# Kernel tuning notes

Hardware: AMD Instinct MI355X
Metric: run time of the kernel (lower is better)

The kernel has to match this reference:

```python
import jax, jax.numpy as jnp
import numpy as np

T, D, E, H, O = 65536, 256, 8, 512, 256
TOP_P = 0.7


def setup_inputs() -> dict:
    key = jax.random.key(0)
    ks = jax.random.split(key, 7)
    s = 0.02
    return {
        "x": jax.random.normal(ks[0], (T, D), dtype=jnp.float32),
        "gate_w": jax.random.normal(ks[1], (D, E), dtype=jnp.float32) * s,
        "gate_b": jnp.zeros((E,), dtype=jnp.float32),
        "w1": jax.random.normal(ks[2], (E, D, H), dtype=jnp.float32) * s,
        "b1": jnp.zeros((E, H), dtype=jnp.float32),
        "w2": jax.random.normal(ks[3], (E, H, O), dtype=jnp.float32) * s,
        "b2": jnp.zeros((E, O), dtype=jnp.float32),
    }


def top_sample(probs, top_p):
    # sort descending, cumsum, keep while cumulative prob <= top_p (always keep top-1)
    order = jnp.argsort(-probs, axis=-1)                       # [T, E]
    probs_sorted = jnp.take_along_axis(probs, order, axis=-1)
    cum = jnp.cumsum(probs_sorted, axis=-1)
    mask = cum <= top_p
    mask = mask.at[:, 0].set(True)
    inv = jnp.argsort(order, axis=-1)                          # unsort permutation
    return jnp.take_along_axis(mask, inv, axis=-1)             # [T, E] bool


def reference(x, gate_w, gate_b, w1, b1, w2, b2):
    logits = x @ gate_w + gate_b                               # [T, E]
    probs = jax.nn.softmax(logits, axis=-1)
    routing_loss = jnp.mean(-jnp.sum(probs * jnp.log(probs + 1e-8), axis=-1))
    expert_mask = top_sample(probs, TOP_P)                     # [T, E]

    # dense per-expert MLP over the entire batch (faithful to original)
    h = jax.nn.gelu(jnp.einsum('td,edh->teh', x, w1) + b1, approximate=False)
    expert_outputs = jnp.einsum('teh,eho->teo', h, w2) + b2    # [T, E, O]

    mask_probs = probs * expert_mask.astype(probs.dtype)
    weights = mask_probs / jnp.sum(mask_probs, axis=-1, keepdims=True)  # [T, E]
    output = jnp.einsum('teo,te->to', expert_outputs, weights)          # [T, O]
    return output, routing_loss
```

## Files before the change

### kernel.cpp

```cpp
#include <hip/hip_runtime.h>
#include <math.h>

#define TT 65536
#define DD 256
#define EE 8
#define HH 512
#define OO 256
#define NN 4096

typedef unsigned int u32;
typedef unsigned short u16;
typedef __attribute__((ext_vector_type(4))) float f32x4;
typedef __attribute__((ext_vector_type(16))) float f32x16;
typedef __attribute__((ext_vector_type(2))) u32 u32x2;
typedef __attribute__((ext_vector_type(4))) u32 u32x4;
typedef __attribute__((ext_vector_type(8))) __bf16 bf16x8;

__device__ __forceinline__ u16 f2bf(float f) {
    u32 u = __builtin_bit_cast(u32, f);
    u32 r = (u + 0x7fffu + ((u >> 16) & 1u)) >> 16;
    return (u16)r;
}

__device__ __forceinline__ u32 cvt_pk_bf16(float lo, float hi) {
    u32 r;
    asm("v_cvt_pk_bf16_f32 %0, %1, %2" : "=v"(r) : "v"(lo), "v"(hi));
    return r;
}

__device__ __forceinline__ bf16x8 ld_frag(const void* p) {
    u32x4 v = *(const u32x4*)p;
    return __builtin_bit_cast(bf16x8, v);
}

__device__ __forceinline__ float gelu_fast(float v) {
    float t = v * v;
    float u = __builtin_fmaf(t, -0.1029479f, -2.3022075f);
    float z = v * u;
    float e = __builtin_amdgcn_exp2f(z);
    return v * __builtin_amdgcn_rcpf(1.0f + e);
}

__global__ __launch_bounds__(256) void k_conv_w1(const float* __restrict__ w1, u16* __restrict__ w1s) {
    int i = blockIdx.x * 256 + threadIdx.x;
    int j = i & 15, l = (i >> 4) & 31, kb = (i >> 9) & 15, nb = i >> 13;
    int n = nb * 32 + l, k = kb * 16 + j;
    int e = n >> 9, h = n & 511;
    w1s[i] = f2bf(w1[(size_t)e * 131072 + (size_t)k * 512 + h]);
}
__global__ __launch_bounds__(256) void k_conv_w2(const float* __restrict__ w2, u16* __restrict__ w2s) {
    int i = blockIdx.x * 256 + threadIdx.x;
    int j = i & 15, l = (i >> 4) & 31, kb2 = (i >> 9) & 255, ob = i >> 17;
    int o = ob * 32 + l, k2 = kb2 * 16 + j;
    int e = k2 >> 9, h = k2 & 511;
    w2s[i] = f2bf(w2[(size_t)e * 131072 + (size_t)h * 256 + o]);
}

__global__ __launch_bounds__(256) void k_gating(const float* __restrict__ x,
                                                const float* __restrict__ gw,
                                                const float* __restrict__ gb,
                                                float* __restrict__ wt,
                                                double* __restrict__ part) {
    __shared__ float gws[DD * EE];
    __shared__ float gbs[EE];
    __shared__ double red[256];
    int tid = threadIdx.x;
    for (int i = tid; i < DD * EE; i += 256) gws[i] = gw[i];
    if (tid < EE) gbs[tid] = gb[tid];
    __syncthreads();

    int t = blockIdx.x * 256 + tid;
    double l[EE];
#pragma unroll
    for (int e = 0; e < EE; ++e) l[e] = (double)gbs[e];

    const f32x4* xr = (const f32x4*)(x + (size_t)t * DD);
    for (int d4 = 0; d4 < DD / 4; ++d4) {
        f32x4 xv = xr[d4];
#pragma unroll
        for (int j = 0; j < 4; ++j) {
            double xs = (double)xv[j];
            int d = d4 * 4 + j;
#pragma unroll
            for (int e = 0; e < EE; ++e) l[e] += xs * (double)gws[d * EE + e];
        }
    }
    double mx = l[0];
#pragma unroll
    for (int e = 1; e < EE; ++e) mx = l[e] > mx ? l[e] : mx;
    double p[EE], s = 0.0;
#pragma unroll
    for (int e = 0; e < EE; ++e) { p[e] = exp(l[e] - mx); s += p[e]; }
    double inv = 1.0 / s;
    double ent = 0.0;
#pragma unroll
    for (int e = 0; e < EE; ++e) { p[e] *= inv; ent += p[e] * log(p[e] + 1e-8); }

    bool mask[EE];
#pragma unroll
    for (int e = 0; e < EE; ++e) {
        double c = 0.0; int rk = 0;
#pragma unroll
        for (int f = 0; f < EE; ++f) {
            bool before = (p[f] > p[e]) || (p[f] == p[e] && f < e);
            if (before) { c += p[f]; rk++; }
        }
        c += p[e];
        mask[e] = (c <= 0.7) || (rk == 0);
    }
    double ms = 0.0;
#pragma unroll
    for (int e = 0; e < EE; ++e) if (mask[e]) ms += p[e];
    double inv2 = 1.0 / ms;
#pragma unroll
    for (int e = 0; e < EE; ++e) wt[(size_t)e * TT + t] = (float)(mask[e] ? p[e] * inv2 : 0.0);

    red[tid] = -ent;
    __syncthreads();
    for (int st = 128; st > 0; st >>= 1) {
        if (tid < st) red[tid] += red[tid + st];
        __syncthreads();
    }
    if (tid == 0) part[blockIdx.x] = red[0];
}

__global__ __launch_bounds__(256) void k_final(const double* __restrict__ part, float* __restrict__ loss) {
    __shared__ double red[256];
    int tid = threadIdx.x;
    red[tid] = part[tid];
    __syncthreads();
    for (int st = 128; st > 0; st >>= 1) {
        if (tid < st) red[tid] += red[tid + st];
        __syncthreads();
    }
    if (tid == 0) loss[0] = (float)(red[0] / (double)TT);
}

__global__ __launch_bounds__(512, 4) void k_moe(const float* __restrict__ x,
                                                const u16* __restrict__ w1s,
                                                const u16* __restrict__ w2s,
                                                const float* __restrict__ b1,
                                                const float* __restrict__ b2,
                                                const float* __restrict__ wtg,
                                                float* __restrict__ out) {
    __shared__ __align__(16) unsigned char smem[67584];
    unsigned char* Hs = smem + 32768;
    float* wts = (float*)(smem + 65536);

    const int tid = threadIdx.x;
    const int wid = tid >> 6;
    const int lane = tid & 63;
    const int l31 = lane & 31;
    const int lg2 = lane >> 5;
    const int t0 = blockIdx.x * 64;
    const int lfrag = l31 * 16 + lg2 * 8;

    {
        const float* xb = x + (size_t)t0 * DD;
#pragma unroll
        for (int i = 0; i < 4; ++i) {
            int L = i * 8192 + tid * 16;
            int row = L >> 9, elem = (L & 511) >> 1;
            const float* src = xb + (size_t)row * DD + elem;
            f32x4 a = *(const f32x4*)src;
            f32x4 b = *(const f32x4*)(src + 4);
            u32x4 o;
            o.x = cvt_pk_bf16(a[0], a[1]); o.y = cvt_pk_bf16(a[2], a[3]);
            o.z = cvt_pk_bf16(b[0], b[1]); o.w = cvt_pk_bf16(b[2], b[3]);
            *(u32x4*)(smem + (L ^ ((row & 15) << 4))) = o;
        }
    }
    wts[tid] = wtg[(size_t)(tid >> 6) * TT + t0 + (tid & 63)];
    __syncthreads();

    f32x16 oacc[2];
    oacc[0] = (f32x16)0.0f;
    oacc[1] = (f32x16)0.0f;

    const int tokA = l31, tokB = 32 + l31;
    const int rbA = tokA * 512 + lg2 * 16, rszA = (tokA & 15) << 4;
    const int rbB = tokB * 512 + lg2 * 16, rszB = (tokB & 15) << 4;

#pragma unroll 1
    for (int c = 0; c < 16; ++c) {
        const int e = c >> 1;
        {
            f32x16 hf0 = (f32x16)0.0f, hf1 = (f32x16)0.0f;
            const u16* w1p = w1s + ((size_t)((c * 8 + wid) * 16)) * 512 + lfrag;
            bf16x8 A[4];
            A[0] = ld_frag(w1p);
            A[1] = ld_frag(w1p + 512);
            A[2] = ld_frag(w1p + 1024);
            A[3] = ld_frag(w1p + 1536);
            __builtin_amdgcn_s_setprio(1);
#pragma unroll 4
            for (int ks = 0; ks < 16; ++ks) {
                bf16x8 ac = A[ks & 3];
                if (ks < 12) A[ks & 3] = ld_frag(w1p + (ks + 4) * 512);
                bf16x8 b0 = ld_frag(smem + ((rbA + ks * 32) ^ rszA));
                bf16x8 b1 = ld_frag(smem + ((rbB + ks * 32) ^ rszB));
                hf0 = __builtin_amdgcn_mfma_f32_32x32x16_bf16(ac, b0, hf0, 0, 0, 0);
                hf1 = __builtin_amdgcn_mfma_f32_32x32x16_bf16(ac, b1, hf1, 0, 0, 0);
            }
            __builtin_amdgcn_s_setprio(0);
            const float* b1p = b1 + c * 256 + wid * 32 + lg2 * 4;
            float wgtA = wts[e * 64 + tokA];
            float wgtB = wts[e * 64 + tokB];
#pragma unroll
            for (int q = 0; q < 4; ++q) {
                f32x4 bb = *(const f32x4*)(b1p + q * 8);
                float g0[4], g1[4];
#pragma unroll
                for (int r = 0; r < 4; ++r) {
                    g0[r] = gelu_fast(hf0[q * 4 + r] + bb[r]) * wgtA;
                    g1[r] = gelu_fast(hf1[q * 4 + r] + bb[r]) * wgtB;
                }
                u32x2 pk0, pk1;
                pk0.x = cvt_pk_bf16(g0[0], g0[1]); pk0.y = cvt_pk_bf16(g0[2], g0[3]);
                pk1.x = cvt_pk_bf16(g1[0], g1[1]); pk1.y = cvt_pk_bf16(g1[2], g1[3]);
                int hb = (wid * 32 + q * 8 + lg2 * 4) * 2;
                *(u32x2*)(Hs + ((tokA * 512 + hb) ^ rszA)) = pk0;
                *(u32x2*)(Hs + ((tokB * 512 + hb) ^ rszB)) = pk1;
            }
        }
        __syncthreads();
        {
            const u16* w2p = w2s + ((size_t)(wid * 256 + c * 16)) * 512 + lfrag;
            bf16x8 B[4];
            B[0] = ld_frag(w2p);
            B[1] = ld_frag(w2p + 512);
            B[2] = ld_frag(w2p + 1024);
            B[3] = ld_frag(w2p + 1536);
            __builtin_amdgcn_s_setprio(1);
#pragma unroll 4
            for (int ks = 0; ks < 16; ++ks) {
                bf16x8 bc = B[ks & 3];
                if (ks < 12) B[ks & 3] = ld_frag(w2p + (ks + 4) * 512);
                bf16x8 A0 = ld_frag(Hs + ((rbA + ks * 32) ^ rszA));
                bf16x8 A1 = ld_frag(Hs + ((rbB + ks * 32) ^ rszB));
                oacc[0] = __builtin_amdgcn_mfma_f32_32x32x16_bf16(A0, bc, oacc[0], 0, 0, 0);
                oacc[1] = __builtin_amdgcn_mfma_f32_32x32x16_bf16(A1, bc, oacc[1], 0, 0, 0);
            }
            __builtin_amdgcn_s_setprio(0);
        }
        __syncthreads();
    }

    {
        int o = wid * 32 + l31;
        float b2v[EE];
#pragma unroll
        for (int e = 0; e < EE; ++e) b2v[e] = b2[e * OO + o];
#pragma unroll
        for (int m = 0; m < 2; ++m) {
#pragma unroll
            for (int r = 0; r < 16; ++r) {
                int tok = m * 32 + (r & 3) + 8 * (r >> 2) + 4 * lg2;
                float wb = 0.f;
#pragma unroll
                for (int e = 0; e < EE; ++e) wb += wts[e * 64 + tok] * b2v[e];
                out[(size_t)(t0 + tok) * OO + o] = oacc[m][r] + wb;
            }
        }
    }
}

extern "C" void kernel_launch(void* const* d_in, const int* in_sizes, int n_in,
                              void* d_out, int out_size, void* d_ws, size_t ws_size,
                              hipStream_t stream) {
    const float* x  = (const float*)d_in[0];
    const float* gw = (const float*)d_in[1];
    const float* gb = (const float*)d_in[2];
    const float* w1 = (const float*)d_in[3];
    const float* b1 = (const float*)d_in[4];
    const float* w2 = (const float*)d_in[5];
    const float* b2 = (const float*)d_in[6];
    float* out = (float*)d_out;

    char* ws = (char*)d_ws;
    u16* w1s    = (u16*)(ws);
    u16* w2s    = (u16*)(ws + 2097152);
    float* wt   = (float*)(ws + 4194304);
    double* prt = (double*)(ws + 6291456);

    k_conv_w1<<<(EE * HH * DD) / 256, 256, 0, stream>>>(w1, w1s);
    k_conv_w2<<<(OO * NN) / 256, 256, 0, stream>>>(w2, w2s);
    k_gating<<<TT / 256, 256, 0, stream>>>(x, gw, gb, wt, prt);
    k_moe<<<TT / 64, 512, 0, stream>>>(x, w1s, w2s, b1, b2, wt, out);
    k_final<<<1, 256, 0, stream>>>(prt, out + (size_t)TT * OO);
}
```

Measured before the change: 368.8 us.

## Sort tokens by expert mask and skip inactive experts per tile

Result: faster. 322.1 us (-12.7%).

```diff
diff --git a/kernel.cpp b/kernel.cpp
--- a/kernel.cpp
+++ b/kernel.cpp
@@ -60,7 +60,10 @@
                                                 const float* __restrict__ gw,
                                                 const float* __restrict__ gb,
                                                 float* __restrict__ wt,
-                                                double* __restrict__ part) {
+                                                double* __restrict__ part,
+                                                u32* __restrict__ maskA,
+                                                u32* __restrict__ rank,
+                                                u32* __restrict__ bins) {
     __shared__ float gws[DD * EE];
     __shared__ float gbs[EE];
     __shared__ double red[256];
@@ -112,8 +115,14 @@
 #pragma unroll
     for (int e = 0; e < EE; ++e) if (mask[e]) ms += p[e];
     double inv2 = 1.0 / ms;
-#pragma unroll
-    for (int e = 0; e < EE; ++e) wt[(size_t)e * TT + t] = (float)(mask[e] ? p[e] * inv2 : 0.0);
+    u32 m = 0;
+#pragma unroll
+    for (int e = 0; e < EE; ++e) {
+        wt[(size_t)e * TT + t] = (float)(mask[e] ? p[e] * inv2 : 0.0);
+        if (mask[e]) m |= (1u << e);
+    }
+    maskA[t] = m;
+    rank[t] = atomicAdd(&bins[m], 1u);
 
     red[tid] = -ent;
     __syncthreads();
@@ -122,6 +131,29 @@
         __syncthreads();
     }
     if (tid == 0) part[blockIdx.x] = red[0];
+}
+
+__global__ __launch_bounds__(256) void k_scan(const u32* __restrict__ bins, u32* __restrict__ base) {
+    __shared__ u32 s[256];
+    int t = threadIdx.x;
+    u32 mine = bins[t];
+    s[t] = mine;
+    __syncthreads();
+    for (int off = 1; off < 256; off <<= 1) {
+        u32 v = (t >= off) ? s[t - off] : 0u;
+        __syncthreads();
+        s[t] += v;
+        __syncthreads();
+    }
+    base[t] = s[t] - mine;
+}
+
+__global__ __launch_bounds__(256) void k_scatter(const u32* __restrict__ maskA,
+                                                 const u32* __restrict__ rank,
+                                                 const u32* __restrict__ base,
+                                                 u32* __restrict__ idx) {
+    int t = blockIdx.x * 256 + threadIdx.x;
+    idx[base[maskA[t]] + rank[t]] = (u32)t;
 }
 
 __global__ __launch_bounds__(256) void k_final(const double* __restrict__ part, float* __restrict__ loss) {
@@ -142,35 +174,42 @@
                                                 const float* __restrict__ b1,
                                                 const float* __restrict__ b2,
                                                 const float* __restrict__ wtg,
+                                                const u32* __restrict__ idxg,
                                                 float* __restrict__ out) {
-    __shared__ __align__(16) unsigned char smem[67584];
+    __shared__ __align__(16) unsigned char smem[68096];
     unsigned char* Hs = smem + 32768;
     float* wts = (float*)(smem + 65536);
+    u32* idxS  = (u32*)(smem + 67584);
+    u32* actS  = (u32*)(smem + 67840);
 
     const int tid = threadIdx.x;
     const int wid = tid >> 6;
     const int lane = tid & 63;
     const int l31 = lane & 31;
     const int lg2 = lane >> 5;
-    const int t0 = blockIdx.x * 64;
     const int lfrag = l31 * 16 + lg2 * 8;
 
+    if (tid < 64) idxS[tid] = idxg[blockIdx.x * 64 + tid];
+    __syncthreads();
+
+#pragma unroll
+    for (int i = 0; i < 4; ++i) {
+        int L = i * 8192 + tid * 16;
+        int row = L >> 9, elem = (L & 511) >> 1;
+        const float* src = x + (size_t)idxS[row] * DD + elem;
+        f32x4 a = *(const f32x4*)src;
+        f32x4 b = *(const f32x4*)(src + 4);
+        u32x4 o;
+        o.x = cvt_pk_bf16(a[0], a[1]); o.y = cvt_pk_bf16(a[2], a[3]);
+        o.z = cvt_pk_bf16(b[0], b[1]); o.w = cvt_pk_bf16(b[2], b[3]);
+        *(u32x4*)(smem + (L ^ ((row & 15) << 4))) = o;
+    }
+    wts[tid] = wtg[(size_t)wid * TT + idxS[lane]];
+    __syncthreads();
     {
-        const float* xb = x + (size_t)t0 * DD;
-#pragma unroll
-        for (int i = 0; i < 4; ++i) {
-            int L = i * 8192 + tid * 16;
-            int row = L >> 9, elem = (L & 511) >> 1;
-            const float* src = xb + (size_t)row * DD + elem;
-            f32x4 a = *(const f32x4*)src;
-            f32x4 b = *(const f32x4*)(src + 4);
-            u32x4 o;
-            o.x = cvt_pk_bf16(a[0], a[1]); o.y = cvt_pk_bf16(a[2], a[3]);
-            o.z = cvt_pk_bf16(b[0], b[1]); o.w = cvt_pk_bf16(b[2], b[3]);
-            *(u32x4*)(smem + (L ^ ((row & 15) << 4))) = o;
-        }
-    }
-    wts[tid] = wtg[(size_t)(tid >> 6) * TT + t0 + (tid & 63)];
+        int av = __any(wts[tid] != 0.0f);
+        if (lane == 0) actS[wid] = (u32)(av != 0);
+    }
     __syncthreads();
 
     f32x16 oacc[2];
@@ -184,6 +223,7 @@
 #pragma unroll 1
     for (int c = 0; c < 16; ++c) {
         const int e = c >> 1;
+        if (!actS[e]) continue;
         {
             f32x16 hf0 = (f32x16)0.0f, hf1 = (f32x16)0.0f;
             const u16* w1p = w1s + ((size_t)((c * 8 + wid) * 16)) * 512 + lfrag;
@@ -259,7 +299,7 @@
                 float wb = 0.f;
 #pragma unroll
                 for (int e = 0; e < EE; ++e) wb += wts[e * 64 + tok] * b2v[e];
-                out[(size_t)(t0 + tok) * OO + o] = oacc[m][r] + wb;
+                out[(size_t)idxS[tok] * OO + o] = oacc[m][r] + wb;
             }
         }
     }
@@ -282,10 +322,18 @@
     u16* w2s    = (u16*)(ws + 2097152);
     float* wt   = (float*)(ws + 4194304);
     double* prt = (double*)(ws + 6291456);
-
+    u32* bins   = (u32*)(ws + 6295552);
+    u32* base   = (u32*)(ws + 6299648);
+    u32* maskA  = (u32*)(ws + 6307840);
+    u32* rank   = (u32*)(ws + 6569984);
+    u32* idx    = (u32*)(ws + 6832128);
+
+    hipMemsetAsync(bins, 0, 1024, stream);
     k_conv_w1<<<(EE * HH * DD) / 256, 256, 0, stream>>>(w1, w1s);
     k_conv_w2<<<(OO * NN) / 256, 256, 0, stream>>>(w2, w2s);
-    k_gating<<<TT / 256, 256, 0, stream>>>(x, gw, gb, wt, prt);
-    k_moe<<<TT / 64, 512, 0, stream>>>(x, w1s, w2s, b1, b2, wt, out);
+    k_gating<<<TT / 256, 256, 0, stream>>>(x, gw, gb, wt, prt, maskA, rank, bins);
+    k_scan<<<1, 256, 0, stream>>>(bins, base);
+    k_scatter<<<TT / 256, 256, 0, stream>>>(maskA, rank, base, idx);
+    k_moe<<<TT / 64, 512, 0, stream>>>(x, w1s, w2s, b1, b2, wt, idx, out);
     k_final<<<1, 256, 0, stream>>>(prt, out + (size_t)TT * OO);
 }
```
